# Performance work log

Measured on AMD Instinct MI355X. Metric: run time of the kernel, lower is better.

Reference implementation:

```python
import jax, jax.numpy as jnp
import numpy as np
import math

B, S, D, H = 4, 1024, 1024, 16
HD = D // H  # 64
EPS = 1e-6
LOG2E = 1.442695041


def setup_inputs() -> dict:
    key = jax.random.key(0)
    ks = jax.random.split(key, 8)
    inputs_q = jax.random.normal(ks[0], (B, S, D), dtype=jnp.float32)
    patch_mask = jnp.zeros((B, S), dtype=bool)
    w_scale = 0.02
    Wq = jax.random.normal(ks[1], (D, D), dtype=jnp.float32) * w_scale
    Wk = jax.random.normal(ks[2], (D, D), dtype=jnp.float32) * w_scale
    Wv = jax.random.normal(ks[3], (D, D), dtype=jnp.float32) * w_scale
    Wo = jax.random.normal(ks[4], (D, D), dtype=jnp.float32) * w_scale
    # RMSNorm scales (torch inits to zero; use random nonzero for a meaningful baseline)
    q_ln_scale = jax.random.uniform(ks[5], (HD,), dtype=jnp.float32, minval=0.5, maxval=1.5)
    k_ln_scale = jax.random.uniform(ks[6], (HD,), dtype=jnp.float32, minval=0.5, maxval=1.5)
    per_dim_scale = jax.random.normal(ks[7], (HD,), dtype=jnp.float32) * 0.1
    return {"inputs_q": inputs_q, "patch_mask": patch_mask, "Wq": Wq, "Wk": Wk,
            "Wv": Wv, "Wo": Wo, "q_ln_scale": q_ln_scale, "k_ln_scale": k_ln_scale,
            "per_dim_scale": per_dim_scale}


def _rope(x, position):
    # x: [b, s, h, hd]; position: [b, s] (float)
    half = HD // 2
    fraction = 2.0 * jnp.arange(half, dtype=x.dtype) / HD
    timescale = 10000.0 ** fraction  # min_timescale=1, max=10000
    sinusoid = position[:, :, None, None] / timescale[None, None, None, :]
    sin, cos = jnp.sin(sinusoid), jnp.cos(sinusoid)
    x1, x2 = jnp.split(x, 2, axis=-1)
    return jnp.concatenate([x1 * cos - x2 * sin, x2 * cos + x1 * sin], axis=-1)


def _rms_norm(x, scale):
    var = jnp.mean(jnp.square(x), axis=-1, keepdims=True)
    return x * jax.lax.rsqrt(var + EPS) * scale


def reference(inputs_q, patch_mask, Wq, Wk, Wv, Wo, q_ln_scale, k_ln_scale, per_dim_scale):
    b, n, _ = inputs_q.shape
    # torch nn.Linear: y = x @ W.T
    q = jnp.einsum('bsd,fd->bsf', inputs_q, Wq).reshape(b, n, H, HD)
    k = jnp.einsum('bsd,fd->bsf', inputs_q, Wk).reshape(b, n, H, HD)
    v = jnp.einsum('bsd,fd->bsf', inputs_q, Wv).reshape(b, n, H, HD)

    num_masked = jnp.sum(patch_mask.astype(jnp.int32), axis=-1, keepdims=True)  # [b,1]
    position = (jnp.arange(n)[None, :] - num_masked).astype(inputs_q.dtype)  # [b,s]

    q = _rope(q, position)
    k = _rope(k, position)
    q = _rms_norm(q, q_ln_scale)
    k = _rms_norm(k, k_ln_scale)
    # per-dim scale (replaces the usual 1/sqrt(d) since SDPA runs with scale=1.0)
    q = q * (LOG2E / math.sqrt(HD) * jax.nn.softplus(per_dim_scale))

    # mask: q_idx >= kv_idx AND kv_idx >= num_masked  -> [b,1,q,kv]
    qi = jnp.arange(n)[None, None, :, None]
    ki = jnp.arange(n)[None, None, None, :]
    attn_mask = (qi >= ki) & (ki >= num_masked[:, None, None])

    scores = jnp.einsum('bqhd,bkhd->bhqk', q, k)  # scale=1.0
    scores = jnp.where(attn_mask, scores, jnp.asarray(-1e30, scores.dtype))
    attn = jax.nn.softmax(scores, axis=-1)
    x = jnp.einsum('bhqk,bkhd->bqhd', attn, v).reshape(b, n, D)
    return jnp.einsum('bsd,fd->bsf', x, Wo)
```

## Files before the change

### kernel.cpp

```cpp
#include <hip/hip_runtime.h>
#include <hip/hip_bf16.h>
#include <stdint.h>

#define B_  4
#define S_  1024
#define D_  1024
#define H_  16
#define HD_ 64

using f32x4  = __attribute__((ext_vector_type(4))) float;
using bf16x8 = __attribute__((ext_vector_type(8))) __bf16;
using bf16x4 = __attribute__((ext_vector_type(4))) __bf16;
using f32x4v = __attribute__((ext_vector_type(4))) float;

__device__ __forceinline__ void g2l16(const void* g, void* l) {
  using gp = const __attribute__((address_space(1))) unsigned int*;
  using lp = __attribute__((address_space(3))) unsigned int*;
  __builtin_amdgcn_global_load_lds((gp)(unsigned long long)g,
                                   (lp)(unsigned int)(unsigned long long)l,
                                   16, 0, 0);
}

__global__ __launch_bounds__(256)
void prep_kernel(const float* __restrict__ X, const float* __restrict__ w0,
                 const float* __restrict__ w1, const float* __restrict__ w2,
                 const float* __restrict__ w3, const unsigned char* __restrict__ mask,
                 const float* __restrict__ qsc, const float* __restrict__ ksc,
                 const float* __restrict__ pds,
                 __bf16* __restrict__ Xb, __bf16* __restrict__ Wqkv,
                 __bf16* __restrict__ Wob, int* __restrict__ nm,
                 float* __restrict__ tab, float* __restrict__ qmul,
                 float* __restrict__ kmul) {
  const int bid = blockIdx.x, tid = threadIdx.x;
  if (bid < 4096) {
    const int i = bid * 1024 + tid * 4;
    f32x4v v = *(const f32x4v*)(X + i);
    bf16x4 o;
    o[0] = (__bf16)v[0]; o[1] = (__bf16)v[1]; o[2] = (__bf16)v[2]; o[3] = (__bf16)v[3];
    *(bf16x4*)(Xb + i) = o;
  } else if (bid < 8192) {
    const int bid2 = bid - 4096;
    const int y = bid2 >> 10;
    const float* src = (y == 0) ? w0 : (y == 1) ? w1 : (y == 2) ? w2 : w3;
    __bf16* dst = (y < 3) ? (Wqkv + (size_t)y * 1048576) : Wob;
    const int i = (bid2 & 1023) * 1024 + tid * 4;
    f32x4v v = *(const f32x4v*)(src + i);
    bf16x4 o;
    o[0] = (__bf16)v[0]; o[1] = (__bf16)v[1]; o[2] = (__bf16)v[2]; o[3] = (__bf16)v[3];
    *(bf16x4*)(dst + i) = o;
  } else if (bid == 8192) {
    const int b = tid >> 6, ln = tid & 63;
    int s = 0;
    for (int i = ln; i < S_; i += 64) s += (mask[b * S_ + i] != 0) ? 1 : 0;
    #pragma unroll
    for (int k = 1; k < 64; k <<= 1) s += __shfl_xor(s, k);
    if (ln == 0) nm[b] = s;
  } else if (bid <= 8321) {
    const int idx = (bid - 8193) * 256 + tid;
    if (idx < 1025 * 32) {
      const int p = idx >> 5, d = idx & 31;
      const float ang = (float)p * exp2f((float)d * -0.41524101186092025f);
      float sn, cs;
      sincosf(ang, &sn, &cs);
      tab[idx * 2]     = sn;
      tab[idx * 2 + 1] = cs;
    }
  } else {
    if (tid < 64) {
      qmul[tid] = qsc[tid] * 0.26017112262570096f * log1pf(expf(pds[tid]));
      kmul[tid] = ksc[tid];
    }
  }
}

template <int MODE>
__global__ __launch_bounds__(256)
void gemm_nt(const __bf16* __restrict__ A, const __bf16* __restrict__ Bm,
             float* __restrict__ Cf, __bf16* __restrict__ Cbf,
             __bf16* __restrict__ Vt, int N, int K) {
  __shared__ __bf16 sA[2][128 * 32];
  __shared__ __bf16 sB[2][128 * 32];
  const int tid = threadIdx.x;
  const int wv = tid >> 6, lane = tid & 63;
  const int row0 = blockIdx.y * 128, col0 = blockIdx.x * 128;
  const int wm = wv >> 1, wn = wv & 1;
  const int c0 = wv * 2, c1 = c0 + 1;
  const int srow = lane >> 2;
  const int scol = (((lane & 3) ^ ((lane >> 3) & 3))) * 8;
  const __bf16* Ab = A + (size_t)(row0 + srow) * K + scol;
  const __bf16* Bb = Bm + (size_t)(col0 + srow) * K + scol;
  const int fr = lane & 15;
  const int fk = ((lane >> 4) ^ ((fr >> 1) & 3)) * 8;

  f32x4 acc[4][4] = {};

#define GSTAGE(buf, k0) do {                                              \
    g2l16(Ab + (size_t)(c0 * 16) * K + (k0), &sA[buf][c0 * 512]);         \
    g2l16(Ab + (size_t)(c1 * 16) * K + (k0), &sA[buf][c1 * 512]);         \
    g2l16(Bb + (size_t)(c0 * 16) * K + (k0), &sB[buf][c0 * 512]);         \
    g2l16(Bb + (size_t)(c1 * 16) * K + (k0), &sB[buf][c1 * 512]);         \
  } while (0)

  GSTAGE(0, 0);
  __syncthreads();
  int cur = 0;
  for (int k0 = 0; k0 < K; k0 += 32) {
    if (k0 + 32 < K) GSTAGE(cur ^ 1, k0 + 32);

    bf16x8 af[4], bfr[4];
    #pragma unroll
    for (int m = 0; m < 4; ++m)
      af[m] = *(const bf16x8*)&sA[cur][(wm * 64 + m * 16 + fr) * 32 + fk];
    #pragma unroll
    for (int n = 0; n < 4; ++n)
      bfr[n] = *(const bf16x8*)&sB[cur][(wn * 64 + n * 16 + fr) * 32 + fk];

    #pragma unroll
    for (int m = 0; m < 4; ++m)
      #pragma unroll
      for (int n = 0; n < 4; ++n)
        acc[m][n] = __builtin_amdgcn_mfma_f32_16x16x32_bf16(af[m], bfr[n], acc[m][n], 0, 0, 0);

    __syncthreads();
    cur ^= 1;
  }
#undef GSTAGE

  const int g4 = (lane >> 4) * 4;
  if (MODE == 0) {
    #pragma unroll
    for (int m = 0; m < 4; ++m)
      #pragma unroll
      for (int n = 0; n < 4; ++n)
        #pragma unroll
        for (int r = 0; r < 4; ++r)
          Cf[(size_t)(row0 + wm * 64 + m * 16 + g4 + r) * N + col0 + wn * 64 + n * 16 + fr] =
              acc[m][n][r];
    return;
  }

  if (col0 >= 2048) {
    #pragma unroll
    for (int m = 0; m < 4; ++m) {
      const int row = row0 + wm * 64 + m * 16 + g4;
      const int bq = row >> 10, s = row & 1023;
      #pragma unroll
      for (int n = 0; n < 4; ++n) {
        const int hd = col0 + wn * 64 + n * 16 + fr - 2048;
        bf16x4 ov;
        #pragma unroll
        for (int r = 0; r < 4; ++r) ov[r] = (__bf16)acc[m][n][r];
        *(bf16x4*)&Vt[(size_t)((bq * H_ + (hd >> 6)) * HD_ + (hd & 63)) * S_ + s] = ov;
      }
    }
  } else {
    #pragma unroll
    for (int m = 0; m < 4; ++m)
      #pragma unroll
      for (int n = 0; n < 4; ++n)
        #pragma unroll
        for (int r = 0; r < 4; ++r)
          Cbf[(size_t)(row0 + wm * 64 + m * 16 + g4 + r) * N + col0 + wn * 64 + n * 16 + fr] =
              (__bf16)acc[m][n][r];
  }
}

__global__ __launch_bounds__(256)
void rope_rms(const __bf16* __restrict__ QKV, __bf16* __restrict__ Qr,
              __bf16* __restrict__ Kr, const float* __restrict__ qmul,
              const float* __restrict__ kmul, const int* __restrict__ nm,
              const float* __restrict__ tab) {
  const int gt = blockIdx.x * 256 + threadIdx.x;
  const int j = gt & 3;
  const int h = (gt >> 2) & 15;
  const int s = (gt >> 6) & 1023;
  const int b = (gt >> 16) & 3;
  const bool isK = gt >= 262144;
  const int dlo = j * 8;

  const __bf16* src = QKV + (size_t)(b * S_ + s) * 3072 + (isK ? 1024 : 0) + h * HD_ + dlo;
  bf16x8 xl = *(const bf16x8*)src;
  bf16x8 xh = *(const bf16x8*)(src + 32);

  const int ip = s - nm[b];
  const int ap = ip < 0 ? -ip : ip;
  const float sgn = ip < 0 ? -1.f : 1.f;
  const float* trow = tab + (size_t)ap * 64 + dlo * 2;
  f32x4v tv[4];
  #pragma unroll
  for (int k = 0; k < 4; ++k) tv[k] = *(const f32x4v*)(trow + k * 4);

  float ol[8], oh[8];
  float ss = 0.f;
  #pragma unroll
  for (int i = 0; i < 8; ++i) {
    const float fl = (float)xl[i];
    const float fh = (float)xh[i];
    const float sn = sgn * tv[i >> 1][(i & 1) * 2];
    const float cs = tv[i >> 1][(i & 1) * 2 + 1];
    ol[i] = fl * cs - fh * sn;
    oh[i] = fh * cs + fl * sn;
    ss += ol[i] * ol[i] + oh[i] * oh[i];
  }
  ss += __shfl_xor(ss, 1);
  ss += __shfl_xor(ss, 2);
  const float rn = rsqrtf(ss * (1.0f / 64.0f) + 1e-6f);

  const float* mul = isK ? kmul : qmul;
  f32x4v ml0 = *(const f32x4v*)(mul + dlo);
  f32x4v ml1 = *(const f32x4v*)(mul + dlo + 4);
  f32x4v mh0 = *(const f32x4v*)(mul + dlo + 32);
  f32x4v mh1 = *(const f32x4v*)(mul + dlo + 36);

  bf16x8 outl, outh;
  #pragma unroll
  for (int i = 0; i < 4; ++i) {
    outl[i]     = (__bf16)(ol[i] * rn * ml0[i]);
    outl[i + 4] = (__bf16)(ol[i + 4] * rn * ml1[i]);
    outh[i]     = (__bf16)(oh[i] * rn * mh0[i]);
    outh[i + 4] = (__bf16)(oh[i + 4] * rn * mh1[i]);
  }
  __bf16* dst = (isK ? Kr : Qr) + ((size_t)(b * H_ + h) * S_ + s) * HD_ + dlo;
  *(bf16x8*)dst = outl;
  *(bf16x8*)(dst + 32) = outh;
}

__global__ __launch_bounds__(256)
void attn_fwd(const __bf16* __restrict__ Qr, const __bf16* __restrict__ Kr,
              const __bf16* __restrict__ Vt, __bf16* __restrict__ Ob,
              const int* __restrict__ nm) {
  const int bid = blockIdx.x;
  const int qblk = 15 - (bid >> 6);
  const int bh = bid & 63;
  const int b = bh >> 4, h = bh & 15;
  const int q0 = qblk * 64;
  const int tid = threadIdx.x, wv = tid >> 6, lane = tid & 63;

  __shared__ __bf16 sK[2][64 * 64];
  __shared__ __bf16 sV[2][64 * 64];
  __shared__ unsigned int sP[4][16 * 32];

  const size_t bhs = (size_t)(b * H_ + h);
  const __bf16* Qh = Qr + bhs * (S_ * HD_);
  const __bf16* Kh = Kr + bhs * (S_ * HD_);
  const __bf16* Vh = Vt + bhs * (HD_ * S_);

  const int fr = lane & 15, g = lane >> 4;
  const int qbase = q0 + wv * 16;
  const int q = qbase + fr;
  unsigned int* sPw = &sP[wv][0];
  const int swz = (fr & 7) << 2;

  bf16x8 qf[2];
  #pragma unroll
  for (int ks = 0; ks < 2; ++ks)
    qf[ks] = *(const bf16x8*)&Qh[(size_t)q * HD_ + ks * 32 + g * 8];

  f32x4 oacc[4] = {};
  float mrun = -3e38f, lrun = 0.f;

  const int nmb = nm[b];
  const int srow = lane >> 3;
  const int ssw = ((lane & 7) ^ srow) * 8;
  const int c0 = wv * 2, c1 = c0 + 1;

#define ASTAGE(buf, kv) do {                                                    \
    g2l16(&Kh[(size_t)((kv) + c0 * 8 + srow) * HD_ + ssw], &sK[buf][c0 * 512]); \
    g2l16(&Kh[(size_t)((kv) + c1 * 8 + srow) * HD_ + ssw], &sK[buf][c1 * 512]); \
    g2l16(&Vh[(size_t)(c0 * 8 + srow) * S_ + (kv) + ssw], &sV[buf][c0 * 512]);  \
    g2l16(&Vh[(size_t)(c1 * 8 + srow) * S_ + (kv) + ssw], &sV[buf][c1 * 512]);  \
  } while (0)

  ASTAGE(0, 0);
  __syncthreads();
  int cur = 0;
  const int kvend = q0 + 64;

  for (int kv0 = 0; kv0 < kvend; kv0 += 64) {
    if (kv0 + 64 < kvend) ASTAGE(cur ^ 1, kv0 + 64);

    f32x4 sacc[4] = {};
    __builtin_amdgcn_s_setprio(1);
    #pragma unroll
    for (int n = 0; n < 4; ++n) {
      const int krow = n * 16 + fr;
      #pragma unroll
      for (int ks = 0; ks < 2; ++ks) {
        bf16x8 kf = *(const bf16x8*)&sK[cur][krow * 64 + ((ks * 32 + g * 8) ^ ((krow & 7) * 8))];
        sacc[n] = __builtin_amdgcn_mfma_f32_16x16x32_bf16(kf, qf[ks], sacc[n], 0, 0, 0);
      }
    }
    __builtin_amdgcn_s_setprio(0);

    const bool fullv = (qbase >= kv0 + 63) && (kv0 >= nmb);
    if (!fullv) {
      #pragma unroll
      for (int n = 0; n < 4; ++n)
        #pragma unroll
        for (int r = 0; r < 4; ++r) {
          const int kv = kv0 + n * 16 + g * 4 + r;
          if (q < kv || kv < nmb) sacc[n][r] = -1e30f;
        }
    }

    float pmax = sacc[0][0];
    #pragma unroll
    for (int n = 0; n < 4; ++n)
      #pragma unroll
      for (int r = 0; r < 4; ++r) pmax = fmaxf(pmax, sacc[n][r]);
    pmax = fmaxf(pmax, __shfl_xor(pmax, 16));
    pmax = fmaxf(pmax, __shfl_xor(pmax, 32));
    if (pmax > mrun + 8.f) {
      const float scl = exp2f(mrun - pmax);
      lrun *= scl;
      #pragma unroll
      for (int nd = 0; nd < 4; ++nd)
        #pragma unroll
        for (int r = 0; r < 4; ++r) oacc[nd][r] *= scl;
      mrun = pmax;
    }
    float ls = 0.f;
    #pragma unroll
    for (int n = 0; n < 4; ++n)
      #pragma unroll
      for (int r = 0; r < 4; ++r) {
        const float p = exp2f(sacc[n][r] - mrun);
        sacc[n][r] = p;
        ls += p;
      }
    ls += __shfl_xor(ls, 16);
    ls += __shfl_xor(ls, 32);
    lrun += ls;

    #pragma unroll
    for (int n = 0; n < 4; ++n) {
      union { unsigned int u; __bf16 hh[2]; } p0, p1;
      p0.hh[0] = (__bf16)sacc[n][0]; p0.hh[1] = (__bf16)sacc[n][1];
      p1.hh[0] = (__bf16)sacc[n][2]; p1.hh[1] = (__bf16)sacc[n][3];
      const unsigned long long pu =
          (unsigned long long)p0.u | ((unsigned long long)p1.u << 32);
      *(unsigned long long*)&sPw[fr * 32 + ((n * 8 + g * 2) ^ swz)] = pu;
    }
    bf16x8 pf[2];
    #pragma unroll
    for (int ks = 0; ks < 2; ++ks)
      pf[ks] = *(const bf16x8*)&sPw[fr * 32 + ((ks * 16 + g * 4) ^ swz)];

    __builtin_amdgcn_s_setprio(1);
    #pragma unroll
    for (int nd = 0; nd < 4; ++nd) {
      const int vrow = nd * 16 + fr;
      #pragma unroll
      for (int ks = 0; ks < 2; ++ks) {
        bf16x8 vf = *(const bf16x8*)&sV[cur][vrow * 64 + ((ks * 32 + g * 8) ^ ((vrow & 7) * 8))];
        oacc[nd] = __builtin_amdgcn_mfma_f32_16x16x32_bf16(vf, pf[ks], oacc[nd], 0, 0, 0);
      }
    }
    __builtin_amdgcn_s_setprio(0);

    __syncthreads();
    cur ^= 1;
  }
#undef ASTAGE

  const float inv = 1.0f / lrun;
  __bf16* orow = Ob + (size_t)(b * S_ + q) * D_ + h * HD_;
  #pragma unroll
  for (int nd = 0; nd < 4; ++nd) {
    bf16x4 ov;
    #pragma unroll
    for (int r = 0; r < 4; ++r) ov[r] = (__bf16)(oacc[nd][r] * inv);
    *(bf16x4*)&orow[nd * 16 + g * 4] = ov;
  }
}

extern "C" void kernel_launch(void* const* d_in, const int* in_sizes, int n_in,
                              void* d_out, int out_size, void* d_ws, size_t ws_size,
                              hipStream_t stream) {
  (void)in_sizes; (void)n_in; (void)out_size; (void)ws_size;
  const float* X  = (const float*)d_in[0];
  const unsigned char* pm = (const unsigned char*)d_in[1];
  const float* Wq = (const float*)d_in[2];
  const float* Wk = (const float*)d_in[3];
  const float* Wv = (const float*)d_in[4];
  const float* Wo = (const float*)d_in[5];
  const float* qs = (const float*)d_in[6];
  const float* ks = (const float*)d_in[7];
  const float* pd = (const float*)d_in[8];
  float* out = (float*)d_out;

  char* ws = (char*)d_ws;
  int*    nm   = (int*)ws;
  __bf16* Wqkv = (__bf16*)(ws + 256);
  __bf16* Wob  = (__bf16*)(ws + 256 + 6291456);
  __bf16* Xb   = (__bf16*)(ws + 8388864);
  __bf16* QKV  = (__bf16*)(ws + 16777472);
  __bf16* Krb  = (__bf16*)(ws + 41943296);
  __bf16* Vtb  = (__bf16*)(ws + 50331904);
  float*  tab  = (float*)(ws + 58720512);
  float*  qmul = (float*)(ws + 58982912);
  float*  kmul = (float*)(ws + 58983168);
  __bf16* Qrb  = Xb;
  __bf16* Obuf = QKV;

  prep_kernel<<<8323, 256, 0, stream>>>(X, Wq, Wk, Wv, Wo, pm, qs, ks, pd,
                                        Xb, Wqkv, Wob, nm, tab, qmul, kmul);

  gemm_nt<1><<<dim3(24, 32), 256, 0, stream>>>(Xb, Wqkv, nullptr, QKV, Vtb, 3072, 1024);

  rope_rms<<<2048, 256, 0, stream>>>(QKV, Qrb, Krb, qmul, kmul, nm, tab);

  attn_fwd<<<1024, 256, 0, stream>>>(Qrb, Krb, Vtb, Obuf, nm);

  gemm_nt<0><<<dim3(8, 32), 256, 0, stream>>>(Obuf, Wob, out, nullptr, nullptr, 1024, 1024);
}
```

Measured before the change: 103.6 us.

## Enlarge attention query tile to 128 rows with two MFMA row tiles per wave

Each attention block now covers 128 query rows instead of 64, and each wave handles two 16-row tiles. Every K and V fragment read from shared memory feeds two MFMAs, which halves per-query LDS reads and global K/V staging. The grid shrinks from 1024 to 512 blocks. That lowers occupancy across CUs and worsens causal load imbalance, since tiles near the diagonal now do more fully masked work. Register pressure also rises from the doubled accumulators.

```diff
diff --git a/kernel.cpp b/kernel.cpp
--- a/kernel.cpp
+++ b/kernel.cpp
@@ -230,15 +230,15 @@
               const __bf16* __restrict__ Vt, __bf16* __restrict__ Ob,
               const int* __restrict__ nm) {
   const int bid = blockIdx.x;
-  const int qblk = 15 - (bid >> 6);
+  const int qblk = 7 - (bid >> 6);
   const int bh = bid & 63;
   const int b = bh >> 4, h = bh & 15;
-  const int q0 = qblk * 64;
+  const int q0 = qblk * 128;
   const int tid = threadIdx.x, wv = tid >> 6, lane = tid & 63;
 
   __shared__ __bf16 sK[2][64 * 64];
   __shared__ __bf16 sV[2][64 * 64];
-  __shared__ unsigned int sP[4][16 * 32];
+  __shared__ unsigned int sP[4][32 * 32];
 
   const size_t bhs = (size_t)(b * H_ + h);
   const __bf16* Qh = Qr + bhs * (S_ * HD_);
@@ -246,18 +246,19 @@
   const __bf16* Vh = Vt + bhs * (HD_ * S_);
 
   const int fr = lane & 15, g = lane >> 4;
-  const int qbase = q0 + wv * 16;
-  const int q = qbase + fr;
+  const int qbase = q0 + wv * 32;
   unsigned int* sPw = &sP[wv][0];
   const int swz = (fr & 7) << 2;
 
-  bf16x8 qf[2];
+  bf16x8 qf[2][2];
   #pragma unroll
-  for (int ks = 0; ks < 2; ++ks)
-    qf[ks] = *(const bf16x8*)&Qh[(size_t)q * HD_ + ks * 32 + g * 8];
-
-  f32x4 oacc[4] = {};
-  float mrun = -3e38f, lrun = 0.f;
+  for (int m = 0; m < 2; ++m)
+    #pragma unroll
+    for (int ks = 0; ks < 2; ++ks)
+      qf[m][ks] = *(const bf16x8*)&Qh[(size_t)(qbase + m * 16 + fr) * HD_ + ks * 32 + g * 8];
+
+  f32x4 oacc[2][4] = {};
+  float mrun[2] = {-3e38f, -3e38f}, lrun[2] = {0.f, 0.f};
 
   const int nmb = nm[b];
   const int srow = lane >> 3;
@@ -274,12 +275,12 @@
   ASTAGE(0, 0);
   __syncthreads();
   int cur = 0;
-  const int kvend = q0 + 64;
+  const int kvend = q0 + 128;
 
   for (int kv0 = 0; kv0 < kvend; kv0 += 64) {
     if (kv0 + 64 < kvend) ASTAGE(cur ^ 1, kv0 + 64);
 
-    f32x4 sacc[4] = {};
+    f32x4 sacc[2][4] = {};
     __builtin_amdgcn_s_setprio(1);
     #pragma unroll
     for (int n = 0; n < 4; ++n) {
@@ -287,7 +288,9 @@
       #pragma unroll
       for (int ks = 0; ks < 2; ++ks) {
         bf16x8 kf = *(const bf16x8*)&sK[cur][krow * 64 + ((ks * 32 + g * 8) ^ ((krow & 7) * 8))];
-        sacc[n] = __builtin_amdgcn_mfma_f32_16x16x32_bf16(kf, qf[ks], sacc[n], 0, 0, 0);
+        #pragma unroll
+        for (int m = 0; m < 2; ++m)
+          sacc[m][n] = __builtin_amdgcn_mfma_f32_16x16x32_bf16(kf, qf[m][ks], sacc[m][n], 0, 0, 0);
       }
     }
     __builtin_amdgcn_s_setprio(0);
@@ -295,56 +298,67 @@
     const bool fullv = (qbase >= kv0 + 63) && (kv0 >= nmb);
     if (!fullv) {
       #pragma unroll
+      for (int m = 0; m < 2; ++m) {
+        const int q = qbase + m * 16 + fr;
+        #pragma unroll
+        for (int n = 0; n < 4; ++n)
+          #pragma unroll
+          for (int r = 0; r < 4; ++r) {
+            const int kv = kv0 + n * 16 + g * 4 + r;
+            if (q < kv || kv < nmb) sacc[m][n][r] = -1e30f;
+          }
+      }
+    }
+
+    #pragma unroll
+    for (int m = 0; m < 2; ++m) {
+      float pmax = sacc[m][0][0];
+      #pragma unroll
       for (int n = 0; n < 4; ++n)
         #pragma unroll
+        for (int r = 0; r < 4; ++r) pmax = fmaxf(pmax, sacc[m][n][r]);
+      pmax = fmaxf(pmax, __shfl_xor(pmax, 16));
+      pmax = fmaxf(pmax, __shfl_xor(pmax, 32));
+      if (pmax > mrun[m] + 8.f) {
+        const float scl = exp2f(mrun[m] - pmax);
+        lrun[m] *= scl;
+        #pragma unroll
+        for (int nd = 0; nd < 4; ++nd)
+          #pragma unroll
+          for (int r = 0; r < 4; ++r) oacc[m][nd][r] *= scl;
+        mrun[m] = pmax;
+      }
+      float ls = 0.f;
+      #pragma unroll
+      for (int n = 0; n < 4; ++n)
+        #pragma unroll
         for (int r = 0; r < 4; ++r) {
-          const int kv = kv0 + n * 16 + g * 4 + r;
-          if (q < kv || kv < nmb) sacc[n][r] = -1e30f;
+          const float p = exp2f(sacc[m][n][r] - mrun[m]);
+          sacc[m][n][r] = p;
+          ls += p;
         }
-    }
-
-    float pmax = sacc[0][0];
-    #pragma unroll
-    for (int n = 0; n < 4; ++n)
-      #pragma unroll
-      for (int r = 0; r < 4; ++r) pmax = fmaxf(pmax, sacc[n][r]);
-    pmax = fmaxf(pmax, __shfl_xor(pmax, 16));
-    pmax = fmaxf(pmax, __shfl_xor(pmax, 32));
-    if (pmax > mrun + 8.f) {
-      const float scl = exp2f(mrun - pmax);
-      lrun *= scl;
-      #pragma unroll
-      for (int nd = 0; nd < 4; ++nd)
-        #pragma unroll
-        for (int r = 0; r < 4; ++r) oacc[nd][r] *= scl;
-      mrun = pmax;
-    }
-    float ls = 0.f;
-    #pragma unroll
-    for (int n = 0; n < 4; ++n)
-      #pragma unroll
-      for (int r = 0; r < 4; ++r) {
-        const float p = exp2f(sacc[n][r] - mrun);
-        sacc[n][r] = p;
-        ls += p;
-      }
-    ls += __shfl_xor(ls, 16);
-    ls += __shfl_xor(ls, 32);
-    lrun += ls;
-
-    #pragma unroll
-    for (int n = 0; n < 4; ++n) {
-      union { unsigned int u; __bf16 hh[2]; } p0, p1;
-      p0.hh[0] = (__bf16)sacc[n][0]; p0.hh[1] = (__bf16)sacc[n][1];
-      p1.hh[0] = (__bf16)sacc[n][2]; p1.hh[1] = (__bf16)sacc[n][3];
-      const unsigned long long pu =
-          (unsigned long long)p0.u | ((unsigned long long)p1.u << 32);
-      *(unsigned long long*)&sPw[fr * 32 + ((n * 8 + g * 2) ^ swz)] = pu;
-    }
-    bf16x8 pf[2];
-    #pragma unroll
-    for (int ks = 0; ks < 2; ++ks)
-      pf[ks] = *(const bf16x8*)&sPw[fr * 32 + ((ks * 16 + g * 4) ^ swz)];
+      ls += __shfl_xor(ls, 16);
+      ls += __shfl_xor(ls, 32);
+      lrun[m] += ls;
+    }
+
+    #pragma unroll
+    for (int m = 0; m < 2; ++m)
+      #pragma unroll
+      for (int n = 0; n < 4; ++n) {
+        union { unsigned int u; __bf16 hh[2]; } p0, p1;
+        p0.hh[0] = (__bf16)sacc[m][n][0]; p0.hh[1] = (__bf16)sacc[m][n][1];
+        p1.hh[0] = (__bf16)sacc[m][n][2]; p1.hh[1] = (__bf16)sacc[m][n][3];
+        const unsigned long long pu =
+            (unsigned long long)p0.u | ((unsigned long long)p1.u << 32);
+        *(unsigned long long*)&sPw[(m * 16 + fr) * 32 + ((n * 8 + g * 2) ^ swz)] = pu;
+      }
+    bf16x8 pf[2][2];
+    #pragma unroll
+    for (int m = 0; m < 2; ++m)
+      #pragma unroll
+      for (int ks = 0; ks < 2; ++ks)
+        pf[m][ks] = *(const bf16x8*)&sPw[(m * 16 + fr) * 32 + ((ks * 16 + g * 4) ^ swz)];
 
     __builtin_amdgcn_s_setprio(1);
     #pragma unroll
@@ -353,7 +367,9 @@
       #pragma unroll
       for (int ks = 0; ks < 2; ++ks) {
         bf16x8 vf = *(const bf16x8*)&sV[cur][vrow * 64 + ((ks * 32 + g * 8) ^ ((vrow & 7) * 8))];
-        oacc[nd] = __builtin_amdgcn_mfma_f32_16x16x32_bf16(vf, pf[ks], oacc[nd], 0, 0, 0);
+        #pragma unroll
+        for (int m = 0; m < 2; ++m)
+          oacc[m][nd] = __builtin_amdgcn_mfma_f32_16x16x32_bf16(vf, pf[m][ks], oacc[m][nd], 0, 0, 0);
       }
     }
     __builtin_amdgcn_s_setprio(0);
@@ -363,14 +379,18 @@
   }
 #undef ASTAGE
 
-  const float inv = 1.0f / lrun;
-  __bf16* orow = Ob + (size_t)(b * S_ + q) * D_ + h * HD_;
   #pragma unroll
-  for (int nd = 0; nd < 4; ++nd) {
-    bf16x4 ov;
-    #pragma unroll
-    for (int r = 0; r < 4; ++r) ov[r] = (__bf16)(oacc[nd][r] * inv);
-    *(bf16x4*)&orow[nd * 16 + g * 4] = ov;
+  for (int m = 0; m < 2; ++m) {
+    const float inv = 1.0f / lrun[m];
+    const int q = qbase + m * 16 + fr;
+    __bf16* orow = Ob + (size_t)(b * S_ + q) * D_ + h * HD_;
+    #pragma unroll
+    for (int nd = 0; nd < 4; ++nd) {
+      bf16x4 ov;
+      #pragma unroll
+      for (int r = 0; r < 4; ++r) ov[r] = (__bf16)(oacc[m][nd][r] * inv);
+      *(bf16x4*)&orow[nd * 16 + g * 4] = ov;
+    }
   }
 }
 
@@ -410,7 +430,7 @@
 
   rope_rms<<<2048, 256, 0, stream>>>(QKV, Qrb, Krb, qmul, kmul, nm, tab);
 
-  attn_fwd<<<1024, 256, 0, stream>>>(Qrb, Krb, Vtb, Obuf, nm);
+  attn_fwd<<<512, 256, 0, stream>>>(Qrb, Krb, Vtb, Obuf, nm);
 
   gemm_nt<0><<<dim3(8, 32), 256, 0, stream>>>(Obuf, Wob, out, nullptr, nullptr, 1024, 1024);
 }
```

After: 113.0 us. 9.1% more time.
